# Performance work log

Hardware: AMD Instinct MI355X
Metric: run time of the kernel (lower is better)

The kernel has to match this reference:

```python
import jax, jax.numpy as jnp
import numpy as np

D_MODEL = 1024
NUM_HEADS = 16
DEPTH = D_MODEL // NUM_HEADS
B, S = 4, 2048


def setup_inputs() -> dict:
    key = jax.random.key(0)
    ks = jax.random.split(key, 13)
    sd = 1.0 / np.sqrt(D_MODEL)
    inp = {
        "q_in": jax.random.normal(ks[0], (B, S, D_MODEL), jnp.float32),
        "k_in": jax.random.normal(ks[1], (B, S, D_MODEL), jnp.float32),
        "v_in": jax.random.normal(ks[2], (B, S, D_MODEL), jnp.float32),
        # binary padding/causal-style mask: 1 = masked position
        "m_in": (jax.random.uniform(ks[3], (B, 1, S, S)) < 0.1).astype(jnp.float32),
        "Wq": jax.random.normal(ks[4], (D_MODEL, D_MODEL), jnp.float32) * sd,
        "bq": jax.random.normal(ks[5], (D_MODEL,), jnp.float32) * 0.01,
        "Wk": jax.random.normal(ks[6], (D_MODEL, D_MODEL), jnp.float32) * sd,
        "bk": jax.random.normal(ks[7], (D_MODEL,), jnp.float32) * 0.01,
        "Wv": jax.random.normal(ks[8], (D_MODEL, D_MODEL), jnp.float32) * sd,
        "bv": jax.random.normal(ks[9], (D_MODEL,), jnp.float32) * 0.01,
        "Wo": jax.random.normal(ks[10], (D_MODEL, D_MODEL), jnp.float32) * sd,
        "bo": jax.random.normal(ks[11], (D_MODEL,), jnp.float32) * 0.01,
    }
    return inp


def _split(t):
    # [B,S,D] -> [B,H,S,depth]
    b, s, _ = t.shape
    return t.reshape(b, s, NUM_HEADS, DEPTH).transpose(0, 2, 1, 3)


def reference(q_in, k_in, v_in, m_in, Wq, bq, Wk, bk, Wv, bv, Wo, bo):
    # torch Linear: x @ W^T + b
    q = _split(q_in @ Wq.T + bq)
    k = _split(k_in @ Wk.T + bk)
    v = _split(v_in @ Wv.T + bv)
    scale = jnp.sqrt(jnp.asarray(DEPTH, jnp.float32))
    scores = jnp.einsum("bhqd,bhkd->bhqk", q, k) / scale
    scores = scores - m_in * 1e6
    attn = jax.nn.softmax(scores, axis=-1)
    out = jnp.einsum("bhqk,bhkd->bhqd", attn, v)  # [B,H,S,depth]
    out = out.transpose(0, 2, 1, 3).reshape(q_in.shape[0], -1, D_MODEL)
    return out @ Wo.T + bo
```

## Files before the change

kernel.cpp:

```cpp
#include <hip/hip_runtime.h>


typedef __bf16 bf16_t;
typedef __bf16 bf16x4 __attribute__((ext_vector_type(4)));
typedef __bf16 bf16x8 __attribute__((ext_vector_type(8)));
typedef float floatx4 __attribute__((ext_vector_type(4)));

#define DMODEL 1024
#define NHEAD  16
#define DEPTH  64
#define BATCH  4
#define SEQ    2048
#define MROWS  (BATCH * SEQ)

#define QSCALE 0.18033688011112042f

#define GLDS16(gaddr, laddr)                                                   \
  __builtin_amdgcn_global_load_lds(                                            \
      (__attribute__((address_space(1))) void*)(gaddr),                        \
      (__attribute__((address_space(3))) void*)(laddr), 16, 0, 0)

__global__ __launch_bounds__(256) void cvt_weights(
    const float* __restrict__ w0, const float* __restrict__ w1,
    const float* __restrict__ w2, const float* __restrict__ w3,
    bf16_t* __restrict__ out) {
  const int n_per4 = (DMODEL * DMODEL) / 4;
  int idx = blockIdx.x * blockDim.x + threadIdx.x;
  int t = idx / n_per4;
  int e4 = idx - t * n_per4;
  const float* src = (t == 0) ? w0 : (t == 1) ? w1 : (t == 2) ? w2 : w3;
  const float sc = (t == 0) ? QSCALE : 1.0f;
  float4 v = ((const float4*)src)[e4];
  bf16_t* dst = out + (size_t)t * (DMODEL * DMODEL) + (size_t)e4 * 4;
  dst[0] = (bf16_t)(v.x * sc); dst[1] = (bf16_t)(v.y * sc);
  dst[2] = (bf16_t)(v.z * sc); dst[3] = (bf16_t)(v.w * sc);
}

__global__ __launch_bounds__(256) void cvt3(
    const float* __restrict__ q, const float* __restrict__ k,
    const float* __restrict__ v, bf16_t* __restrict__ dst) {
  const size_t n8 = (size_t)MROWS * DMODEL / 8;
  size_t i = (size_t)blockIdx.x * blockDim.x + threadIdx.x;
  int t = (int)(i / n8);
  size_t e = i - (size_t)t * n8;
  const float* src = (t == 0) ? q : (t == 1) ? k : v;
  const float4* s = (const float4*)(src + e * 8);
  float4 f0 = s[0], f1 = s[1];
  bf16x8 o;
  o[0] = (bf16_t)f0.x; o[1] = (bf16_t)f0.y; o[2] = (bf16_t)f0.z; o[3] = (bf16_t)f0.w;
  o[4] = (bf16_t)f1.x; o[5] = (bf16_t)f1.y; o[6] = (bf16_t)f1.z; o[7] = (bf16_t)f1.w;
  *(bf16x8*)(dst + i * 8) = o;
}

__global__ __launch_bounds__(256) void mask_prepack(
    const float* __restrict__ m, unsigned int* __restrict__ M32) {
  size_t t = (size_t)blockIdx.x * blockDim.x + threadIdx.x;
  int lane = t & 63;
  int it = (t >> 6) & 31;
  int g  = (t >> 11) & 63;
  int b  = (int)(t >> 17);
  int quad = lane >> 4, l16 = lane & 15;
  unsigned int bits = 0;
#pragma unroll
  for (int mi = 0; mi < 2; mi++) {
#pragma unroll
    for (int r = 0; r < 4; r++) {
      const int q = g * 32 + mi * 16 + quad * 4 + r;
      const float* row = m + ((size_t)b * SEQ + q) * SEQ + it * 64 + l16;
#pragma unroll
      for (int ni = 0; ni < 4; ni++) {
        if (row[ni * 16] == 0.f) bits |= 1u << ((mi * 4 + r) * 4 + ni);
      }
    }
  }
  M32[t] = bits;
}

__global__ __launch_bounds__(256) void gemm_qkv(
    const bf16_t* __restrict__ Abf3, const bf16_t* __restrict__ Wbf,
    const float* __restrict__ bq, const float* __restrict__ bk,
    const float* __restrict__ bv, bf16_t* __restrict__ Qh,
    bf16_t* __restrict__ Kh, bf16_t* __restrict__ Vth) {
  __shared__ __align__(16) bf16_t As[128 * 32];
  __shared__ __align__(16) bf16_t Bs[128 * 32];
  const int K = DMODEL;
  const int tid = threadIdx.x;
  const int lane = tid & 63;
  const int w = tid >> 6;
  const int quad = lane >> 4;
  const int l16 = lane & 15;
  const int wm = w & 1, wn = w >> 1;
  const int z = blockIdx.z;

  const bf16_t* A = Abf3 + (size_t)z * MROWS * DMODEL;
  const bf16_t* Bt = Wbf + (size_t)z * DMODEL * DMODEL;
  const float* bias = (z == 0) ? bq : (z == 1) ? bk : bv;
  const float bias_scale = (z == 0) ? QSCALE : 1.0f;
  bf16_t* Ov = (z == 0) ? Qh : (z == 1) ? Kh : Vth;

  const int lin = blockIdx.x + 8 * blockIdx.y;
  const int c = lin & 7;
  const int j = lin >> 3;
  const int n0 = (j & 7) * 128;
  const int m0 = ((j >> 3) * 8 + c) * 128;

  const int r4 = lane >> 2;
  const int c4 = (lane & 3) ^ (r4 & 3);
  const bf16_t* Ag = A + (size_t)(m0 + w * 32 + r4) * K + c4 * 8;
  const bf16_t* Bg = Bt + (size_t)(n0 + w * 32 + r4) * K + c4 * 8;
  char* AsB = (char*)As + (w * 32) * 64;
  char* BsB = (char*)Bs + (w * 32) * 64;

  floatx4 acc[4][4] = {};

  for (int kk = 0; kk < K; kk += 32) {
    __syncthreads();
    GLDS16(Ag + kk, AsB);
    GLDS16(Ag + kk + (size_t)16 * K, AsB + 16 * 64);
    GLDS16(Bg + kk, BsB);
    GLDS16(Bg + kk + (size_t)16 * K, BsB + 16 * 64);
    __syncthreads();

    bf16x8 af[4], bfr[4];
#pragma unroll
    for (int mi = 0; mi < 4; mi++) {
      const char* Arow = (const char*)As + (wm * 64 + mi * 16 + l16) * 64;
      af[mi] = *(const bf16x8*)(Arow + ((quad ^ (l16 & 3)) * 16));
    }
#pragma unroll
    for (int ni = 0; ni < 4; ni++) {
      const char* Brow = (const char*)Bs + (wn * 64 + ni * 16 + l16) * 64;
      bfr[ni] = *(const bf16x8*)(Brow + ((quad ^ (l16 & 3)) * 16));
    }
#pragma unroll
    for (int mi = 0; mi < 4; mi++)
#pragma unroll
      for (int ni = 0; ni < 4; ni++)
        acc[mi][ni] = __builtin_amdgcn_mfma_f32_16x16x32_bf16(af[mi], bfr[ni], acc[mi][ni], 0, 0, 0);
  }

#pragma unroll
  for (int ni = 0; ni < 4; ni++) {
    const int col = n0 + wn * 64 + ni * 16 + l16;
    const float bvl = bias_scale * bias[col];
    const int hh = col >> 6, d = col & (DEPTH - 1);
#pragma unroll
    for (int mi = 0; mi < 4; mi++) {
#pragma unroll
      for (int r = 0; r < 4; r++) {
        const int row = m0 + wm * 64 + mi * 16 + quad * 4 + r;
        const float val = acc[mi][ni][r] + bvl;
        const int bb = row >> 11, s = row & (SEQ - 1);
        if (z != 2) {
          Ov[((((size_t)bb * NHEAD + hh) * SEQ + s) << 6) + d] = (bf16_t)val;
        } else {
          Ov[(((size_t)bb * NHEAD + hh) * DEPTH + d) * SEQ + s] = (bf16_t)val;
        }
      }
    }
  }
}

__global__ __launch_bounds__(256) void gemm_wo(
    const bf16_t* __restrict__ A, const bf16_t* __restrict__ Bt,
    const float* __restrict__ bias, float* __restrict__ Ov,
    int M, int N, int K) {
  __shared__ __align__(16) bf16_t As[128 * 32];
  __shared__ __align__(16) bf16_t Bs[128 * 32];
  const int tid = threadIdx.x;
  const int lane = tid & 63;
  const int w = tid >> 6;
  const int quad = lane >> 4;
  const int l16 = lane & 15;
  const int wm = w & 1, wn = w >> 1;

  const int lin = blockIdx.x + 8 * blockIdx.y;
  const int c = lin & 7;
  const int j = lin >> 3;
  const int n0 = (j & 7) * 128;
  const int m0 = ((j >> 3) * 8 + c) * 128;

  const int r4 = lane >> 2;
  const int c4 = (lane & 3) ^ (r4 & 3);
  const bf16_t* Ag = A + (size_t)(m0 + w * 32 + r4) * K + c4 * 8;
  const bf16_t* Bg = Bt + (size_t)(n0 + w * 32 + r4) * K + c4 * 8;
  char* AsB = (char*)As + (w * 32) * 64;
  char* BsB = (char*)Bs + (w * 32) * 64;

  floatx4 acc[4][4] = {};

  for (int kk = 0; kk < K; kk += 32) {
    __syncthreads();
    GLDS16(Ag + kk, AsB);
    GLDS16(Ag + kk + (size_t)16 * K, AsB + 16 * 64);
    GLDS16(Bg + kk, BsB);
    GLDS16(Bg + kk + (size_t)16 * K, BsB + 16 * 64);
    __syncthreads();

    bf16x8 af[4], bfr[4];
#pragma unroll
    for (int mi = 0; mi < 4; mi++) {
      const char* Arow = (const char*)As + (wm * 64 + mi * 16 + l16) * 64;
      af[mi] = *(const bf16x8*)(Arow + ((quad ^ (l16 & 3)) * 16));
    }
#pragma unroll
    for (int ni = 0; ni < 4; ni++) {
      const char* Brow = (const char*)Bs + (wn * 64 + ni * 16 + l16) * 64;
      bfr[ni] = *(const bf16x8*)(Brow + ((quad ^ (l16 & 3)) * 16));
    }
#pragma unroll
    for (int mi = 0; mi < 4; mi++)
#pragma unroll
      for (int ni = 0; ni < 4; ni++)
        acc[mi][ni] = __builtin_amdgcn_mfma_f32_16x16x32_bf16(af[mi], bfr[ni], acc[mi][ni], 0, 0, 0);
  }

#pragma unroll
  for (int ni = 0; ni < 4; ni++) {
    const int col = n0 + wn * 64 + ni * 16 + l16;
    const float bv = bias[col];
#pragma unroll
    for (int mi = 0; mi < 4; mi++)
#pragma unroll
      for (int r = 0; r < 4; r++) {
        const int row = m0 + wm * 64 + mi * 16 + quad * 4 + r;
        Ov[(size_t)row * N + col] = acc[mi][ni][r] + bv;
      }
  }
}

__global__ __launch_bounds__(256) void attn_kernel(
    const bf16_t* __restrict__ Qh, const bf16_t* __restrict__ Kh,
    const bf16_t* __restrict__ Vt, const unsigned int* __restrict__ M32,
    bf16_t* __restrict__ O) {
  const int lane = threadIdx.x & 63;
  const int w = __builtin_amdgcn_readfirstlane(threadIdx.x >> 6);
  const int quad = lane >> 4;
  const int l16 = lane & 15;

  const int lin = blockIdx.x + 16 * blockIdx.y + 256 * blockIdx.z;
  const int x8 = lin & 7;
  const int kk = lin >> 3;
  const int qt = kk & 15;
  const int p = ((kk >> 4) << 3) | x8;
  const int h = p & 15;
  const int b = p >> 4;
  const int q0 = qt * 128;

  const bf16_t* Qb = Qh + ((size_t)b * NHEAD + h) * SEQ * DEPTH;
  const bf16_t* Kb = Kh + ((size_t)b * NHEAD + h) * SEQ * DEPTH;
  const bf16_t* Vb = Vt + ((size_t)b * NHEAD + h) * DEPTH * SEQ;
  const unsigned int* Mw =
      M32 + ((size_t)b * 64 + (qt * 4 + w)) * 32 * 64 + lane;

  __shared__ __align__(16) bf16_t Ksm[64 * 64];
  __shared__ __align__(16) bf16_t Vsm[64 * 64];
  __shared__ __align__(16) bf16_t Pw[4][32][68];

  const int r8 = lane >> 3;
  const int c8 = (lane & 7) ^ r8;
  const bf16_t* Kg = Kb + (size_t)(w * 16 + r8) * DEPTH + c8 * 8;
  const bf16_t* Vg = Vb + (size_t)(w * 16 + r8) * SEQ + c8 * 8;
  char* KsB = (char*)Ksm + (w * 16) * 128;
  char* VsB = (char*)Vsm + (w * 16) * 128;

  bf16x8 aq[2][2];
#pragma unroll
  for (int mi = 0; mi < 2; mi++) {
    const bf16_t* qp = Qb + (size_t)(q0 + w * 32 + mi * 16 + l16) * DEPTH + quad * 8;
    aq[mi][0] = *(const bf16x8*)qp;
    aq[mi][1] = *(const bf16x8*)(qp + 32);
  }

  floatx4 acco[2][4] = {};
  float lsum[2][4] = {};
  const int swz = l16 & 7;

  for (int it = 0; it < SEQ / 64; ++it) {
    const int sk = it * 64;
    __syncthreads();
    GLDS16(Kg + (size_t)sk * DEPTH, KsB);
    GLDS16(Kg + (size_t)sk * DEPTH + 8 * DEPTH, KsB + 8 * 128);
    GLDS16(Vg + sk, VsB);
    GLDS16(Vg + sk + (size_t)8 * SEQ, VsB + 8 * 128);
    __syncthreads();

    const unsigned int mword = Mw[it * 64];

#pragma unroll
    for (int ni = 0; ni < 4; ni++) {
      const char* Krow = (const char*)Ksm + (ni * 16 + l16) * 128;
      bf16x8 k0 = *(const bf16x8*)(Krow + ((quad ^ swz) * 16));
      bf16x8 k1 = *(const bf16x8*)(Krow + (((4 + quad) ^ swz) * 16));
      floatx4 s[2];
#pragma unroll
      for (int mi = 0; mi < 2; mi++) {
        floatx4 z = {};
        z = __builtin_amdgcn_mfma_f32_16x16x32_bf16(aq[mi][0], k0, z, 0, 0, 0);
        s[mi] = __builtin_amdgcn_mfma_f32_16x16x32_bf16(aq[mi][1], k1, z, 0, 0, 0);
      }
#pragma unroll
      for (int mi = 0; mi < 2; mi++) {
#pragma unroll
        for (int r = 0; r < 4; r++) {
          float pv = __builtin_amdgcn_exp2f(s[mi][r]);
          const int idx = (mi * 4 + r) * 4 + ni;
          const int km = ((int)(mword << (31 - idx))) >> 31;
          pv = __int_as_float(__float_as_int(pv) & km);
          lsum[mi][r] += pv;
          Pw[w][mi * 16 + quad * 4 + r][ni * 16 + l16] = (bf16_t)pv;
        }
      }
    }

    bf16x8 pa[2][2];
#pragma unroll
    for (int mi = 0; mi < 2; mi++) {
#pragma unroll
      for (int kb = 0; kb < 2; kb++) {
        const bf16_t* pp = &Pw[w][mi * 16 + l16][kb * 32 + quad * 8];
        bf16x4 lo = *(const bf16x4*)pp;
        bf16x4 hi = *(const bf16x4*)(pp + 4);
        pa[mi][kb] = __builtin_shufflevector(lo, hi, 0, 1, 2, 3, 4, 5, 6, 7);
      }
    }
#pragma unroll
    for (int ni = 0; ni < 4; ni++) {
      const char* Vrow = (const char*)Vsm + (ni * 16 + l16) * 128;
#pragma unroll
      for (int kb = 0; kb < 2; kb++) {
        bf16x8 vb = *(const bf16x8*)(Vrow + ((((kb * 4) + quad) ^ swz) * 16));
#pragma unroll
        for (int mi = 0; mi < 2; mi++)
          acco[mi][ni] = __builtin_amdgcn_mfma_f32_16x16x32_bf16(pa[mi][kb], vb, acco[mi][ni], 0, 0, 0);
      }
    }
  }

  float inv_l[2][4];
#pragma unroll
  for (int mi = 0; mi < 2; mi++)
#pragma unroll
    for (int r = 0; r < 4; r++) {
      float s = lsum[mi][r];
      s += __shfl_xor(s, 1);
      s += __shfl_xor(s, 2);
      s += __shfl_xor(s, 4);
      s += __shfl_xor(s, 8);
      inv_l[mi][r] = __frcp_rn(s);
    }

#pragma unroll
  for (int mi = 0; mi < 2; mi++)
#pragma unroll
    for (int ni = 0; ni < 4; ni++)
#pragma unroll
      for (int r = 0; r < 4; r++) {
        const int s = q0 + w * 32 + mi * 16 + quad * 4 + r;
        const int d = h * DEPTH + ni * 16 + l16;
        O[((size_t)b * SEQ + s) * DMODEL + d] = (bf16_t)(acco[mi][ni][r] * inv_l[mi][r]);
      }
}

extern "C" void kernel_launch(void* const* d_in, const int* in_sizes, int n_in,
                              void* d_out, int out_size, void* d_ws, size_t ws_size,
                              hipStream_t stream) {
  const float* q_in = (const float*)d_in[0];
  const float* k_in = (const float*)d_in[1];
  const float* v_in = (const float*)d_in[2];
  const float* m_in = (const float*)d_in[3];
  const float* Wq = (const float*)d_in[4];
  const float* bq = (const float*)d_in[5];
  const float* Wk = (const float*)d_in[6];
  const float* bk = (const float*)d_in[7];
  const float* Wv = (const float*)d_in[8];
  const float* bv = (const float*)d_in[9];
  const float* Wo = (const float*)d_in[10];
  const float* bo = (const float*)d_in[11];

  char* ws = (char*)d_ws;
  const size_t MB = 1024 * 1024;
  bf16_t* wbf  = (bf16_t*)ws;
  bf16_t* Abf3 = (bf16_t*)(ws + 8 * MB);
  bf16_t* Obuf = (bf16_t*)(ws + 8 * MB);
  bf16_t* Qh   = (bf16_t*)(ws + 56 * MB);
  bf16_t* Kh   = (bf16_t*)(ws + 72 * MB);
  bf16_t* Vth  = (bf16_t*)(ws + 88 * MB);
  unsigned int* M32 = (unsigned int*)(ws + 104 * MB);

  cvt_weights<<<(4 * (DMODEL * DMODEL / 4)) / 256, 256, 0, stream>>>(
      Wq, Wk, Wv, Wo, wbf);
  cvt3<<<(3 * (MROWS * DMODEL / 8)) / 256, 256, 0, stream>>>(
      q_in, k_in, v_in, Abf3);
  mask_prepack<<<(BATCH * 64 * 32 * 64) / 256, 256, 0, stream>>>(m_in, M32);

  dim3 gqkv(8, 64, 3);
  gemm_qkv<<<gqkv, 256, 0, stream>>>(Abf3, wbf, bq, bk, bv, Qh, Kh, Vth);

  dim3 ga(SEQ / 128, NHEAD, BATCH);
  attn_kernel<<<ga, 256, 0, stream>>>(Qh, Kh, Vth, M32, Obuf);

  dim3 gg(8, 64);
  gemm_wo<<<gg, 256, 0, stream>>>(
      Obuf, wbf + 3 * (size_t)DMODEL * DMODEL, bo, (float*)d_out,
      MROWS, DMODEL, DMODEL);
}
```

Before: 427.0 us.

## Use 32x32 MFMA with transposed scores to keep P in registers

The attention kernel now computes S^T with 32x32x16 bf16 MFMAs, so the score fragment layout matches the A-operand layout needed for the PV MFMA. This removes the per-tile LDS round trip for the P matrix and its extra reads and writes. K rows are permuted at load time to line up the layouts. The mask prepack is rewritten to match the new bit order and to use float4 loads. Launch bounds request 4 blocks per CU, and row sums are combined through a small LDS array at the end.

```diff
diff --git a/kernel.cpp b/kernel.cpp
--- a/kernel.cpp
+++ b/kernel.cpp
@@ -5,6 +5,7 @@
 typedef __bf16 bf16x4 __attribute__((ext_vector_type(4)));
 typedef __bf16 bf16x8 __attribute__((ext_vector_type(8)));
 typedef float floatx4 __attribute__((ext_vector_type(4)));
+typedef float floatx16 __attribute__((ext_vector_type(16)));
 
 #define DMODEL 1024
 #define NHEAD  16
@@ -55,22 +56,25 @@
 __global__ __launch_bounds__(256) void mask_prepack(
     const float* __restrict__ m, unsigned int* __restrict__ M32) {
   size_t t = (size_t)blockIdx.x * blockDim.x + threadIdx.x;
-  int lane = t & 63;
-  int it = (t >> 6) & 31;
-  int g  = (t >> 11) & 63;
+  int lane = (int)(t & 63);
+  int it = (int)((t >> 6) & 31);
+  int g  = (int)((t >> 11) & 63);
   int b  = (int)(t >> 17);
-  int quad = lane >> 4, l16 = lane & 15;
+  int q  = g * 32 + (lane & 31);
+  int hi = lane >> 5;
+  const float* row = m + ((size_t)b * SEQ + q) * SEQ + it * 64;
   unsigned int bits = 0;
 #pragma unroll
-  for (int mi = 0; mi < 2; mi++) {
-#pragma unroll
-    for (int r = 0; r < 4; r++) {
-      const int q = g * 32 + mi * 16 + quad * 4 + r;
-      const float* row = m + ((size_t)b * SEQ + q) * SEQ + it * 64 + l16;
-#pragma unroll
-      for (int ni = 0; ni < 4; ni++) {
-        if (row[ni * 16] == 0.f) bits |= 1u << ((mi * 4 + r) * 4 + ni);
-      }
+  for (int kb = 0; kb < 2; kb++) {
+#pragma unroll
+    for (int rc = 0; rc < 4; rc++) {
+      const int base = kb * 32 + 16 * (rc >> 1) + 8 * hi + 4 * (rc & 1);
+      const float4 mv = *(const float4*)(row + base);
+      const int bit0 = kb * 16 + rc * 4;
+      if (mv.x == 0.f) bits |= 1u << (bit0 + 0);
+      if (mv.y == 0.f) bits |= 1u << (bit0 + 1);
+      if (mv.z == 0.f) bits |= 1u << (bit0 + 2);
+      if (mv.w == 0.f) bits |= 1u << (bit0 + 3);
     }
   }
   M32[t] = bits;
@@ -229,22 +233,22 @@
   }
 }
 
-__global__ __launch_bounds__(256) void attn_kernel(
+__global__ __launch_bounds__(256, 4) void attn_kernel(
     const bf16_t* __restrict__ Qh, const bf16_t* __restrict__ Kh,
     const bf16_t* __restrict__ Vt, const unsigned int* __restrict__ M32,
     bf16_t* __restrict__ O) {
   const int lane = threadIdx.x & 63;
   const int w = __builtin_amdgcn_readfirstlane(threadIdx.x >> 6);
-  const int quad = lane >> 4;
-  const int l16 = lane & 15;
+  const int l31 = lane & 31;
+  const int hi = lane >> 5;
 
   const int lin = blockIdx.x + 16 * blockIdx.y + 256 * blockIdx.z;
   const int x8 = lin & 7;
   const int kk = lin >> 3;
   const int qt = kk & 15;
-  const int p = ((kk >> 4) << 3) | x8;
-  const int h = p & 15;
-  const int b = p >> 4;
+  const int bh = ((kk >> 4) << 3) | x8;
+  const int h = bh & 15;
+  const int b = bh >> 4;
   const int q0 = qt * 128;
 
   const bf16_t* Qb = Qh + ((size_t)b * NHEAD + h) * SEQ * DEPTH;
@@ -255,111 +259,96 @@
 
   __shared__ __align__(16) bf16_t Ksm[64 * 64];
   __shared__ __align__(16) bf16_t Vsm[64 * 64];
-  __shared__ __align__(16) bf16_t Pw[4][32][68];
+  __shared__ float Lsm[4][32];
 
   const int r8 = lane >> 3;
   const int c8 = (lane & 7) ^ r8;
-  const bf16_t* Kg = Kb + (size_t)(w * 16 + r8) * DEPTH + c8 * 8;
-  const bf16_t* Vg = Vb + (size_t)(w * 16 + r8) * SEQ + c8 * 8;
-  char* KsB = (char*)Ksm + (w * 16) * 128;
-  char* VsB = (char*)Vsm + (w * 16) * 128;
-
-  bf16x8 aq[2][2];
-#pragma unroll
-  for (int mi = 0; mi < 2; mi++) {
-    const bf16_t* qp = Qb + (size_t)(q0 + w * 32 + mi * 16 + l16) * DEPTH + quad * 8;
-    aq[mi][0] = *(const bf16x8*)qp;
-    aq[mi][1] = *(const bf16x8*)(qp + 32);
-  }
-
-  floatx4 acco[2][4] = {};
-  float lsum[2][4] = {};
-  const int swz = l16 & 7;
+  const int i1 = w * 16 + r8;
+  const int i2 = i1 + 8;
+  const int lo1 = i1 & 31, lo2 = i2 & 31;
+  const int s1 = (i1 & 32) | ((lo1 & ~12) | ((lo1 & 4) << 1) | ((lo1 & 8) >> 1));
+  const int s2 = (i2 & 32) | ((lo2 & ~12) | ((lo2 & 4) << 1) | ((lo2 & 8) >> 1));
+  const bf16_t* Kg1 = Kb + (size_t)s1 * DEPTH + c8 * 8;
+  const bf16_t* Kg2 = Kb + (size_t)s2 * DEPTH + c8 * 8;
+  const bf16_t* Vg  = Vb + (size_t)(w * 16 + r8) * SEQ + c8 * 8;
+  const int woff = (w * 16) * 128;
+
+  bf16x8 aq[4];
+  {
+    const bf16_t* qp = Qb + (size_t)(q0 + w * 32 + l31) * DEPTH + hi * 8;
+#pragma unroll
+    for (int t = 0; t < 4; t++) aq[t] = *(const bf16x8*)(qp + t * 16);
+  }
+
+  floatx16 acco[2] = {};
+  float lsum = 0.f;
+  const int kxor = l31 & 7;
 
   for (int it = 0; it < SEQ / 64; ++it) {
     const int sk = it * 64;
     __syncthreads();
-    GLDS16(Kg + (size_t)sk * DEPTH, KsB);
-    GLDS16(Kg + (size_t)sk * DEPTH + 8 * DEPTH, KsB + 8 * 128);
-    GLDS16(Vg + sk, VsB);
-    GLDS16(Vg + sk + (size_t)8 * SEQ, VsB + 8 * 128);
+    {
+      char* KsB = (char*)Ksm + woff;
+      char* VsB = (char*)Vsm + woff;
+      GLDS16(Kg1 + (size_t)sk * DEPTH, KsB);
+      GLDS16(Kg2 + (size_t)sk * DEPTH, KsB + 8 * 128);
+      GLDS16(Vg + sk, VsB);
+      GLDS16(Vg + sk + (size_t)8 * SEQ, VsB + 8 * 128);
+    }
     __syncthreads();
 
     const unsigned int mword = Mw[it * 64];
 
 #pragma unroll
-    for (int ni = 0; ni < 4; ni++) {
-      const char* Krow = (const char*)Ksm + (ni * 16 + l16) * 128;
-      bf16x8 k0 = *(const bf16x8*)(Krow + ((quad ^ swz) * 16));
-      bf16x8 k1 = *(const bf16x8*)(Krow + (((4 + quad) ^ swz) * 16));
-      floatx4 s[2];
-#pragma unroll
-      for (int mi = 0; mi < 2; mi++) {
-        floatx4 z = {};
-        z = __builtin_amdgcn_mfma_f32_16x16x32_bf16(aq[mi][0], k0, z, 0, 0, 0);
-        s[mi] = __builtin_amdgcn_mfma_f32_16x16x32_bf16(aq[mi][1], k1, z, 0, 0, 0);
-      }
-#pragma unroll
-      for (int mi = 0; mi < 2; mi++) {
-#pragma unroll
-        for (int r = 0; r < 4; r++) {
-          float pv = __builtin_amdgcn_exp2f(s[mi][r]);
-          const int idx = (mi * 4 + r) * 4 + ni;
-          const int km = ((int)(mword << (31 - idx))) >> 31;
-          pv = __int_as_float(__float_as_int(pv) & km);
-          lsum[mi][r] += pv;
-          Pw[w][mi * 16 + quad * 4 + r][ni * 16 + l16] = (bf16_t)pv;
+    for (int kb = 0; kb < 2; kb++) {
+      floatx16 s = {};
+      const char* Krow = (const char*)Ksm + (kb * 32 + l31) * 128;
+#pragma unroll
+      for (int t = 0; t < 4; t++) {
+        bf16x8 kf = *(const bf16x8*)(Krow + (((2 * t + hi) ^ kxor) * 16));
+        s = __builtin_amdgcn_mfma_f32_32x32x16_bf16(kf, aq[t], s, 0, 0, 0);
+      }
+      float pv[16];
+#pragma unroll
+      for (int r = 0; r < 16; r++) {
+        float e = __builtin_amdgcn_exp2f(s[r]);
+        const int idx = kb * 16 + r;
+        const int km = ((int)(mword << (31 - idx))) >> 31;
+        e = __int_as_float(__float_as_int(e) & km);
+        lsum += e;
+        pv[r] = e;
+      }
+#pragma unroll
+      for (int mh = 0; mh < 2; mh++) {
+        bf16x8 pa;
+#pragma unroll
+        for (int j = 0; j < 8; j++) pa[j] = (bf16_t)pv[mh * 8 + j];
+        const int m = kb * 2 + mh;
+#pragma unroll
+        for (int n = 0; n < 2; n++) {
+          const char* Vrow = (const char*)Vsm + (n * 32 + l31) * 128;
+          bf16x8 vf = *(const bf16x8*)(Vrow + (((2 * m + hi) ^ kxor) * 16));
+          acco[n] = __builtin_amdgcn_mfma_f32_32x32x16_bf16(pa, vf, acco[n], 0, 0, 0);
         }
       }
     }
-
-    bf16x8 pa[2][2];
-#pragma unroll
-    for (int mi = 0; mi < 2; mi++) {
-#pragma unroll
-      for (int kb = 0; kb < 2; kb++) {
-        const bf16_t* pp = &Pw[w][mi * 16 + l16][kb * 32 + quad * 8];
-        bf16x4 lo = *(const bf16x4*)pp;
-        bf16x4 hi = *(const bf16x4*)(pp + 4);
-        pa[mi][kb] = __builtin_shufflevector(lo, hi, 0, 1, 2, 3, 4, 5, 6, 7);
-      }
-    }
-#pragma unroll
-    for (int ni = 0; ni < 4; ni++) {
-      const char* Vrow = (const char*)Vsm + (ni * 16 + l16) * 128;
-#pragma unroll
-      for (int kb = 0; kb < 2; kb++) {
-        bf16x8 vb = *(const bf16x8*)(Vrow + ((((kb * 4) + quad) ^ swz) * 16));
-#pragma unroll
-        for (int mi = 0; mi < 2; mi++)
-          acco[mi][ni] = __builtin_amdgcn_mfma_f32_16x16x32_bf16(pa[mi][kb], vb, acco[mi][ni], 0, 0, 0);
-      }
-    }
-  }
-
-  float inv_l[2][4];
-#pragma unroll
-  for (int mi = 0; mi < 2; mi++)
-#pragma unroll
-    for (int r = 0; r < 4; r++) {
-      float s = lsum[mi][r];
-      s += __shfl_xor(s, 1);
-      s += __shfl_xor(s, 2);
-      s += __shfl_xor(s, 4);
-      s += __shfl_xor(s, 8);
-      inv_l[mi][r] = __frcp_rn(s);
-    }
-
-#pragma unroll
-  for (int mi = 0; mi < 2; mi++)
-#pragma unroll
-    for (int ni = 0; ni < 4; ni++)
-#pragma unroll
-      for (int r = 0; r < 4; r++) {
-        const int s = q0 + w * 32 + mi * 16 + quad * 4 + r;
-        const int d = h * DEPTH + ni * 16 + l16;
-        O[((size_t)b * SEQ + s) * DMODEL + d] = (bf16_t)(acco[mi][ni][r] * inv_l[mi][r]);
-      }
+  }
+
+  float tot = lsum + __shfl_xor(lsum, 32);
+  if (lane < 32) Lsm[w][l31] = __frcp_rn(tot);
+  __syncthreads();
+
+#pragma unroll
+  for (int r = 0; r < 16; r++) {
+    const int qr = (r & 3) + 8 * (r >> 2) + 4 * hi;
+    const float inv = Lsm[w][qr];
+    const size_t srow = (size_t)q0 + w * 32 + qr;
+#pragma unroll
+    for (int n = 0; n < 2; n++) {
+      const int d = h * DEPTH + n * 32 + l31;
+      O[((size_t)b * SEQ + srow) * DMODEL + d] = (bf16_t)(acco[n][r] * inv);
+    }
+  }
 }
 
 extern "C" void kernel_launch(void* const* d_in, const int* in_sizes, int n_in,
```

New measurement: 413.0 us. 3.3% less time.
